# Kernel tuning notes

Hardware: AMD Instinct MI355X
Metric: run time of the kernel (lower is better)

Reference implementation:

```python
import jax, jax.numpy as jnp
import numpy as np

PATCH = 16  # conv kernel size == stride


def _patch_embed(im, W, b):
    # im: (B, C, H, W) NCHW; W: (hidden, C, s, s); returns (B, h, w, hidden)
    out = jax.lax.conv_general_dilated(
        im, W, window_strides=(PATCH, PATCH), padding='VALID',
        dimension_numbers=('NCHW', 'OIHW', 'NCHW'))
    out = out + b[None, :, None, None]
    return jnp.transpose(out, (0, 2, 3, 1))  # (B, h, w, hidden)


def setup_inputs() -> dict:
    key = jax.random.key(0)
    k1, k2, k3, k4 = jax.random.split(key, 4)
    B, C, H, Wd = 64, 3, 224, 224
    hidden = 384
    x = jax.random.normal(k1, (B, C, H, Wd), dtype=jnp.float32)
    y = jax.random.normal(k2, (B, C, H, Wd), dtype=jnp.float32)
    fan_in = C * PATCH * PATCH
    bound = 1.0 / np.sqrt(fan_in)
    W = jax.random.uniform(k3, (hidden, C, PATCH, PATCH), dtype=jnp.float32,
                           minval=-bound, maxval=bound)
    b = jax.random.uniform(k4, (hidden,), dtype=jnp.float32,
                           minval=-bound, maxval=bound)
    return {'x': x, 'y': y, 'W': W, 'b': b}


def reference(x, y, W, b):
    B = x.shape[0]
    xp = _patch_embed(x, W, b)  # (B, h, w, C)
    yp = _patch_embed(y, W, b)  # (B, h, w, C)
    h, w = xp.shape[1], xp.shape[2]
    logp = jax.nn.log_softmax(xp, axis=-1)          # (B, h, w, C)
    q = jax.lax.stop_gradient(jax.nn.softmax(yp, axis=-1))  # detached targets
    # CE[i, j] = mean over (h, w) of -(q_j * logp_i).sum(-1)
    # Faithful factorization of the (B, B, h, w, C) broadcast in the original.
    CE = -jnp.einsum('ihwc,jhwc->ij', logp, q) / (h * w)  # (B, B)
    close = jnp.trace(CE) / B
    far = (CE.sum() - jnp.trace(CE)) / (B * B - B)
    return close / far
```

## Files before the change

### kernel.cpp

```cpp
#include <hip/hip_runtime.h>

#define HID   384
#define K_PE  768
#define IMGST 150528

typedef unsigned short ushort_t;
using f32x4  = __attribute__((ext_vector_type(4))) float;
using short8 = __attribute__((ext_vector_type(8))) short;

__device__ __forceinline__ unsigned bfpack(float lo, float hi) {
    union { float f; unsigned u; } a, b; a.f = lo; b.f = hi;
    unsigned ra = (a.u + 0x7fffu + ((a.u >> 16) & 1u)) >> 16;
    unsigned rb = (b.u + 0x7fffu + ((b.u >> 16) & 1u)) & 0xffff0000u;
    return ra | rb;
}

__global__ __launch_bounds__(256) void prep(const float* __restrict__ W,
                                            ushort_t* __restrict__ Wfrag,
                                            float* __restrict__ scal) {
    const int t = blockIdx.x * 256 + threadIdx.x;
    if (t < 4) scal[t] = 0.f;
    const int n  = t / 96;
    const int ko = t % 96;
    const float4 a = *(const float4*)(W + (size_t)n * K_PE + ko * 8);
    const float4 b = *(const float4*)(W + (size_t)n * K_PE + ko * 8 + 4);
    uint4 p;
    p.x = bfpack(a.x, a.y); p.y = bfpack(a.z, a.w);
    p.z = bfpack(b.x, b.y); p.w = bfpack(b.z, b.w);
    const int nt   = n >> 4;
    const int kc   = ko >> 2;
    const int lane = (ko & 3) * 16 + (n & 15);
    ((uint4*)Wfrag)[(nt * 24 + kc) * 64 + lane] = p;
}

__global__ __launch_bounds__(512, 2) void pe_all(
    const float* __restrict__ xin, const float* __restrict__ yin,
    const ushort_t* __restrict__ Wfrag, const float* __restrict__ bias,
    float* __restrict__ scal, float* __restrict__ out) {
    const int p  = blockIdx.x;
    const int pi = p / 14;
    const int pj = p - pi * 14;

    __shared__ __align__(16) ushort_t Asx[2][64 * 64];
    __shared__ __align__(16) ushort_t Asy[2][64 * 64];
    __shared__ float Smx[8][32], Ssx[8][32], Smy[8][32], Ssy[8][32];
    __shared__ float LcL[2][HID], LcQ[2][HID];
    __shared__ float sT[8], sS[8];

    const int tid  = threadIdx.x;
    const int wave = tid >> 6;
    const int lane = tid & 63;
    const int lm   = lane & 15;
    const int lq   = lane >> 4;
    const int mg   = wave >> 2;
    const int nw   = wave & 3;
    const int wn   = nw * 96;

    const int sm = tid >> 3;
    const int qt = tid & 7;
    const float* abx = xin + (size_t)sm * IMGST + pi * 3584 + pj * 16;
    const float* aby = yin + (size_t)sm * IMGST + pi * 3584 + pj * 16;
    const int awoff = sm * 64 + ((qt ^ (sm & 7)) * 8);

    int ard[2][2];
#pragma unroll
    for (int ks = 0; ks < 2; ++ks)
#pragma unroll
        for (int mi = 0; mi < 2; ++mi)
            ard[ks][mi] = (mg * 32 + mi * 16 + lm) * 64 +
                          (((ks * 4 + lq) ^ (lm & 7)) * 8);

    const ushort_t* bbase = Wfrag + (size_t)lane * 8;

    f32x4 accx[2][6] = {};
    f32x4 accy[2][6] = {};

#define STAGE(KB, BUF)                                                       \
    {                                                                        \
        const int k0  = (KB) + qt * 8;                                       \
        const int off = (k0 >> 8) * 50176 + (((k0 >> 4) & 15) * 224) + (k0 & 15); \
        float4 f0 = *(const float4*)(abx + off);                             \
        float4 f1 = *(const float4*)(abx + off + 4);                         \
        float4 g0 = *(const float4*)(aby + off);                             \
        float4 g1 = *(const float4*)(aby + off + 4);                         \
        uint4 px, py;                                                        \
        px.x = bfpack(f0.x, f0.y); px.y = bfpack(f0.z, f0.w);                \
        px.z = bfpack(f1.x, f1.y); px.w = bfpack(f1.z, f1.w);                \
        py.x = bfpack(g0.x, g0.y); py.y = bfpack(g0.z, g0.w);                \
        py.z = bfpack(g1.x, g1.y); py.w = bfpack(g1.z, g1.w);                \
        *(uint4*)&Asx[BUF][awoff] = px;                                      \
        *(uint4*)&Asy[BUF][awoff] = py;                                      \
    }

    STAGE(0, 0)
    __syncthreads();

    for (int kbi = 0; kbi < 12; ++kbi) {
        const int cur = kbi & 1;
        if (kbi < 11) STAGE(kbi * 64 + 64, cur ^ 1)
#pragma unroll
        for (int ks = 0; ks < 2; ++ks) {
            short8 bfr[6], afx[2], afy[2];
#pragma unroll
            for (int ni = 0; ni < 6; ++ni)
                bfr[ni] = *(const short8*)(bbase +
                          (size_t)(((nw * 6 + ni) * 24 + kbi * 2 + ks) * 64) * 8);
#pragma unroll
            for (int mi = 0; mi < 2; ++mi) {
                afx[mi] = *(const short8*)&Asx[cur][ard[ks][mi]];
                afy[mi] = *(const short8*)&Asy[cur][ard[ks][mi]];
            }
#pragma unroll
            for (int mi = 0; mi < 2; ++mi)
#pragma unroll
                for (int ni = 0; ni < 6; ++ni) {
                    accx[mi][ni] = __builtin_amdgcn_mfma_f32_16x16x32_bf16(
                        afx[mi], bfr[ni], accx[mi][ni], 0, 0, 0);
                    accy[mi][ni] = __builtin_amdgcn_mfma_f32_16x16x32_bf16(
                        afy[mi], bfr[ni], accy[mi][ni], 0, 0, 0);
                }
        }
        __syncthreads();
    }
#undef STAGE

#pragma unroll
    for (int ni = 0; ni < 6; ++ni) {
        const float bv = bias[wn + ni * 16 + lm];
#pragma unroll
        for (int mi = 0; mi < 2; ++mi)
#pragma unroll
            for (int r = 0; r < 4; ++r) {
                accx[mi][ni][r] += bv;
                accy[mi][ni][r] += bv;
            }
    }

    float mx[2][4], my_[2][4];
#pragma unroll
    for (int mi = 0; mi < 2; ++mi)
#pragma unroll
        for (int r = 0; r < 4; ++r) {
            float a = accx[mi][0][r], b = accy[mi][0][r];
#pragma unroll
            for (int ni = 1; ni < 6; ++ni) {
                a = fmaxf(a, accx[mi][ni][r]);
                b = fmaxf(b, accy[mi][ni][r]);
            }
            mx[mi][r] = a; my_[mi][r] = b;
        }
#pragma unroll
    for (int off = 1; off < 16; off <<= 1)
#pragma unroll
        for (int mi = 0; mi < 2; ++mi)
#pragma unroll
            for (int r = 0; r < 4; ++r) {
                mx[mi][r]  = fmaxf(mx[mi][r],  __shfl_xor(mx[mi][r],  off));
                my_[mi][r] = fmaxf(my_[mi][r], __shfl_xor(my_[mi][r], off));
            }
    if (lm == 0)
#pragma unroll
        for (int mi = 0; mi < 2; ++mi)
#pragma unroll
            for (int r = 0; r < 4; ++r) {
                Smx[wave][mi * 16 + lq * 4 + r] = mx[mi][r];
                Smy[wave][mi * 16 + lq * 4 + r] = my_[mi][r];
            }
    __syncthreads();
#pragma unroll
    for (int mi = 0; mi < 2; ++mi)
#pragma unroll
        for (int r = 0; r < 4; ++r) {
            const int row = mi * 16 + lq * 4 + r;
            mx[mi][r]  = fmaxf(fmaxf(Smx[mg * 4 + 0][row], Smx[mg * 4 + 1][row]),
                               fmaxf(Smx[mg * 4 + 2][row], Smx[mg * 4 + 3][row]));
            my_[mi][r] = fmaxf(fmaxf(Smy[mg * 4 + 0][row], Smy[mg * 4 + 1][row]),
                               fmaxf(Smy[mg * 4 + 2][row], Smy[mg * 4 + 3][row]));
        }

    float sx[2][4], sy[2][4];
#pragma unroll
    for (int mi = 0; mi < 2; ++mi)
#pragma unroll
        for (int r = 0; r < 4; ++r) {
            float a = 0.f, b = 0.f;
#pragma unroll
            for (int ni = 0; ni < 6; ++ni) {
                a += __expf(accx[mi][ni][r] - mx[mi][r]);
                b += __expf(accy[mi][ni][r] - my_[mi][r]);
            }
            sx[mi][r] = a; sy[mi][r] = b;
        }
#pragma unroll
    for (int off = 1; off < 16; off <<= 1)
#pragma unroll
        for (int mi = 0; mi < 2; ++mi)
#pragma unroll
            for (int r = 0; r < 4; ++r) {
                sx[mi][r] += __shfl_xor(sx[mi][r], off);
                sy[mi][r] += __shfl_xor(sy[mi][r], off);
            }
    if (lm == 0)
#pragma unroll
        for (int mi = 0; mi < 2; ++mi)
#pragma unroll
            for (int r = 0; r < 4; ++r) {
                Ssx[wave][mi * 16 + lq * 4 + r] = sx[mi][r];
                Ssy[wave][mi * 16 + lq * 4 + r] = sy[mi][r];
            }
    __syncthreads();
#pragma unroll
    for (int mi = 0; mi < 2; ++mi)
#pragma unroll
        for (int r = 0; r < 4; ++r) {
            const int row = mi * 16 + lq * 4 + r;
            const float ssx = Ssx[mg * 4 + 0][row] + Ssx[mg * 4 + 1][row] +
                              Ssx[mg * 4 + 2][row] + Ssx[mg * 4 + 3][row];
            const float ssy = Ssy[mg * 4 + 0][row] + Ssy[mg * 4 + 1][row] +
                              Ssy[mg * 4 + 2][row] + Ssy[mg * 4 + 3][row];
            sx[mi][r] = mx[mi][r] + __logf(ssx);
            sy[mi][r] = 1.f / ssy;
        }

    float T = 0.f;
    float cL[6], cQ[6];
#pragma unroll
    for (int ni = 0; ni < 6; ++ni) { cL[ni] = 0.f; cQ[ni] = 0.f; }
#pragma unroll
    for (int mi = 0; mi < 2; ++mi)
#pragma unroll
        for (int r = 0; r < 4; ++r) {
            const float sh  = sx[mi][r];
            const float m   = my_[mi][r];
            const float inv = sy[mi][r];
#pragma unroll
            for (int ni = 0; ni < 6; ++ni) {
                const float lp = accx[mi][ni][r] - sh;
                const float qv = __expf(accy[mi][ni][r] - m) * inv;
                T += lp * qv;
                cL[ni] += lp;
                cQ[ni] += qv;
            }
        }
#pragma unroll
    for (int ni = 0; ni < 6; ++ni) {
        cL[ni] += __shfl_xor(cL[ni], 16); cL[ni] += __shfl_xor(cL[ni], 32);
        cQ[ni] += __shfl_xor(cQ[ni], 16); cQ[ni] += __shfl_xor(cQ[ni], 32);
    }
    if (lq == 0)
#pragma unroll
        for (int ni = 0; ni < 6; ++ni) {
            LcL[mg][wn + ni * 16 + lm] = cL[ni];
            LcQ[mg][wn + ni * 16 + lm] = cQ[ni];
        }
#pragma unroll
    for (int off = 32; off > 0; off >>= 1) T += __shfl_xor(T, off);
    if (lane == 0) sT[wave] = T;
    __syncthreads();

    float sp = 0.f;
    if (tid < HID) {
        const float L = LcL[0][tid] + LcL[1][tid];
        const float Q = LcQ[0][tid] + LcQ[1][tid];
        sp = L * Q;
    }
#pragma unroll
    for (int off = 32; off > 0; off >>= 1) sp += __shfl_xor(sp, off);
    if (lane == 0) sS[wave] = sp;
    __syncthreads();

    if (tid == 0) {
        float Tb = sT[0] + sT[1] + sT[2] + sT[3] + sT[4] + sT[5] + sT[6] + sT[7];
        float Sb = sS[0] + sS[1] + sS[2] + sS[3] + sS[4] + sS[5] + sS[6] + sS[7];
        atomicAdd(&scal[0], Tb);
        atomicAdd(&scal[1], Sb);
        __threadfence();
        int old = atomicAdd((int*)&scal[3], 1);
        if (old == (int)gridDim.x - 1) {
            float Tt = atomicAdd(&scal[0], 0.f);
            float St = atomicAdd(&scal[1], 0.f);
            out[0] = 63.f * Tt / (St - Tt);
        }
    }
}

extern "C" void kernel_launch(void* const* d_in, const int* in_sizes, int n_in,
                              void* d_out, int out_size, void* d_ws, size_t ws_size,
                              hipStream_t stream) {
    const float* x = (const float*)d_in[0];
    const float* y = (const float*)d_in[1];
    const float* W = (const float*)d_in[2];
    const float* b = (const float*)d_in[3];
    float* out = (float*)d_out;

    float*    scal  = (float*)d_ws;
    ushort_t* Wfrag = (ushort_t*)(scal + 16);

    prep<<<144, 256, 0, stream>>>(W, Wfrag, scal);
    pe_all<<<196, 512, 0, stream>>>(x, y, Wfrag, b, scal, out);
}
```

Measured before the change: 145.6 us.

## Split batch across blocks with atomic column sums and a final dot kernel

The batch of 64 images is split into four groups of 16, giving a 196x4 grid of 256-thread blocks instead of 196 blocks of 512 threads. Each block adds its per-patch column sums of log-probabilities and targets into global arrays with atomics. A third kernel then computes the sum of their products and the final ratio. This raises parallelism and occupancy across the device, at the cost of global atomic traffic, an extra launch, and reloading the weight fragments four times as often.

```diff
diff --git a/kernel.cpp b/kernel.cpp
--- a/kernel.cpp
+++ b/kernel.cpp
@@ -3,6 +3,7 @@
 #define HID   384
 #define K_PE  768
 #define IMGST 150528
+#define NCOLS 75264
 
 typedef unsigned short ushort_t;
 using f32x4  = __attribute__((ext_vector_type(4))) float;
@@ -17,79 +18,78 @@
 
 __global__ __launch_bounds__(256) void prep(const float* __restrict__ W,
                                             ushort_t* __restrict__ Wfrag,
-                                            float* __restrict__ scal) {
+                                            float* __restrict__ scal,
+                                            float* __restrict__ Lsum,
+                                            float* __restrict__ Qsum) {
     const int t = blockIdx.x * 256 + threadIdx.x;
     if (t < 4) scal[t] = 0.f;
-    const int n  = t / 96;
-    const int ko = t % 96;
-    const float4 a = *(const float4*)(W + (size_t)n * K_PE + ko * 8);
-    const float4 b = *(const float4*)(W + (size_t)n * K_PE + ko * 8 + 4);
-    uint4 p;
-    p.x = bfpack(a.x, a.y); p.y = bfpack(a.z, a.w);
-    p.z = bfpack(b.x, b.y); p.w = bfpack(b.z, b.w);
-    const int nt   = n >> 4;
-    const int kc   = ko >> 2;
-    const int lane = (ko & 3) * 16 + (n & 15);
-    ((uint4*)Wfrag)[(nt * 24 + kc) * 64 + lane] = p;
-}
-
-__global__ __launch_bounds__(512, 2) void pe_all(
+    if (t < NCOLS / 4) {
+        ((float4*)Lsum)[t] = float4{0.f, 0.f, 0.f, 0.f};
+        ((float4*)Qsum)[t] = float4{0.f, 0.f, 0.f, 0.f};
+    }
+    if (t < 36864) {
+        const int n  = t / 96;
+        const int ko = t % 96;
+        const float4 a = *(const float4*)(W + (size_t)n * K_PE + ko * 8);
+        const float4 b = *(const float4*)(W + (size_t)n * K_PE + ko * 8 + 4);
+        uint4 p;
+        p.x = bfpack(a.x, a.y); p.y = bfpack(a.z, a.w);
+        p.z = bfpack(b.x, b.y); p.w = bfpack(b.z, b.w);
+        const int nt   = n >> 4;
+        const int kc   = ko >> 2;
+        const int lane = (ko & 3) * 16 + (n & 15);
+        ((uint4*)Wfrag)[(nt * 24 + kc) * 64 + lane] = p;
+    }
+}
+
+__global__ __launch_bounds__(256, 4) void pe_all(
     const float* __restrict__ xin, const float* __restrict__ yin,
     const ushort_t* __restrict__ Wfrag, const float* __restrict__ bias,
-    float* __restrict__ scal, float* __restrict__ out) {
+    float* __restrict__ scal, float* __restrict__ Lsum,
+    float* __restrict__ Qsum) {
     const int p  = blockIdx.x;
+    const int ig = blockIdx.y;
     const int pi = p / 14;
     const int pj = p - pi * 14;
 
-    __shared__ __align__(16) ushort_t Asx[2][64 * 64];
-    __shared__ __align__(16) ushort_t Asy[2][64 * 64];
-    __shared__ float Smx[8][32], Ssx[8][32], Smy[8][32], Ssy[8][32];
-    __shared__ float LcL[2][HID], LcQ[2][HID];
-    __shared__ float sT[8], sS[8];
+    __shared__ __align__(16) ushort_t As[2][2][16 * 64];
+    __shared__ float Smx[4][16], Ssx[4][16], Smy[4][16], Ssy[4][16];
+    __shared__ float sT[4];
 
     const int tid  = threadIdx.x;
     const int wave = tid >> 6;
     const int lane = tid & 63;
     const int lm   = lane & 15;
     const int lq   = lane >> 4;
-    const int mg   = wave >> 2;
-    const int nw   = wave & 3;
-    const int wn   = nw * 96;
-
-    const int sm = tid >> 3;
+    const int wn   = wave * 96;
+
+    const int z  = tid >> 7;
+    const int sm = (tid >> 3) & 15;
     const int qt = tid & 7;
-    const float* abx = xin + (size_t)sm * IMGST + pi * 3584 + pj * 16;
-    const float* aby = yin + (size_t)sm * IMGST + pi * 3584 + pj * 16;
-    const int awoff = sm * 64 + ((qt ^ (sm & 7)) * 8);
-
-    int ard[2][2];
+    const float* ab = (z ? yin : xin) +
+                      (size_t)(ig * 16 + sm) * IMGST + pi * 3584 + pj * 16;
+    ushort_t* awp = &As[z][0][sm * 64 + ((qt ^ (sm & 7)) * 8)];
+
+    int ard[2];
 #pragma unroll
     for (int ks = 0; ks < 2; ++ks)
-#pragma unroll
-        for (int mi = 0; mi < 2; ++mi)
-            ard[ks][mi] = (mg * 32 + mi * 16 + lm) * 64 +
-                          (((ks * 4 + lq) ^ (lm & 7)) * 8);
+        ard[ks] = lm * 64 + (((ks * 4 + lq) ^ (lm & 7)) * 8);
 
     const ushort_t* bbase = Wfrag + (size_t)lane * 8;
 
-    f32x4 accx[2][6] = {};
-    f32x4 accy[2][6] = {};
+    f32x4 accx[6] = {};
+    f32x4 accy[6] = {};
 
 #define STAGE(KB, BUF)                                                       \
     {                                                                        \
         const int k0  = (KB) + qt * 8;                                       \
         const int off = (k0 >> 8) * 50176 + (((k0 >> 4) & 15) * 224) + (k0 & 15); \
-        float4 f0 = *(const float4*)(abx + off);                             \
-        float4 f1 = *(const float4*)(abx + off + 4);                         \
-        float4 g0 = *(const float4*)(aby + off);                             \
-        float4 g1 = *(const float4*)(aby + off + 4);                         \
-        uint4 px, py;                                                        \
+        float4 f0 = *(const float4*)(ab + off);                              \
+        float4 f1 = *(const float4*)(ab + off + 4);                          \
+        uint4 px;                                                            \
         px.x = bfpack(f0.x, f0.y); px.y = bfpack(f0.z, f0.w);                \
         px.z = bfpack(f1.x, f1.y); px.w = bfpack(f1.z, f1.w);                \
-        py.x = bfpack(g0.x, g0.y); py.y = bfpack(g0.z, g0.w);                \
-        py.z = bfpack(g1.x, g1.y); py.w = bfpack(g1.z, g1.w);                \
-        *(uint4*)&Asx[BUF][awoff] = px;                                      \
-        *(uint4*)&Asy[BUF][awoff] = py;                                      \
+        *(uint4*)(awp + (BUF) * 1024) = px;                                  \
     }
 
     STAGE(0, 0)
@@ -100,25 +100,20 @@
         if (kbi < 11) STAGE(kbi * 64 + 64, cur ^ 1)
 #pragma unroll
         for (int ks = 0; ks < 2; ++ks) {
-            short8 bfr[6], afx[2], afy[2];
+            short8 bfr[6];
 #pragma unroll
             for (int ni = 0; ni < 6; ++ni)
                 bfr[ni] = *(const short8*)(bbase +
-                          (size_t)(((nw * 6 + ni) * 24 + kbi * 2 + ks) * 64) * 8);
-#pragma unroll
-            for (int mi = 0; mi < 2; ++mi) {
-                afx[mi] = *(const short8*)&Asx[cur][ard[ks][mi]];
-                afy[mi] = *(const short8*)&Asy[cur][ard[ks][mi]];
+                          (size_t)(((wave * 6 + ni) * 24 + kbi * 2 + ks) * 64) * 8);
+            short8 afx = *(const short8*)&As[0][cur][ard[ks]];
+            short8 afy = *(const short8*)&As[1][cur][ard[ks]];
+#pragma unroll
+            for (int ni = 0; ni < 6; ++ni) {
+                accx[ni] = __builtin_amdgcn_mfma_f32_16x16x32_bf16(
+                    afx, bfr[ni], accx[ni], 0, 0, 0);
+                accy[ni] = __builtin_amdgcn_mfma_f32_16x16x32_bf16(
+                    afy, bfr[ni], accy[ni], 0, 0, 0);
             }
-#pragma unroll
-            for (int mi = 0; mi < 2; ++mi)
-#pragma unroll
-                for (int ni = 0; ni < 6; ++ni) {
-                    accx[mi][ni] = __builtin_amdgcn_mfma_f32_16x16x32_bf16(
-                        afx[mi], bfr[ni], accx[mi][ni], 0, 0, 0);
-                    accy[mi][ni] = __builtin_amdgcn_mfma_f32_16x16x32_bf16(
-                        afy[mi], bfr[ni], accy[mi][ni], 0, 0, 0);
-                }
         }
         __syncthreads();
     }
@@ -128,120 +123,98 @@
     for (int ni = 0; ni < 6; ++ni) {
         const float bv = bias[wn + ni * 16 + lm];
 #pragma unroll
-        for (int mi = 0; mi < 2; ++mi)
-#pragma unroll
-            for (int r = 0; r < 4; ++r) {
-                accx[mi][ni][r] += bv;
-                accy[mi][ni][r] += bv;
-            }
-    }
-
-    float mx[2][4], my_[2][4];
-#pragma unroll
-    for (int mi = 0; mi < 2; ++mi)
-#pragma unroll
-        for (int r = 0; r < 4; ++r) {
-            float a = accx[mi][0][r], b = accy[mi][0][r];
-#pragma unroll
-            for (int ni = 1; ni < 6; ++ni) {
-                a = fmaxf(a, accx[mi][ni][r]);
-                b = fmaxf(b, accy[mi][ni][r]);
-            }
-            mx[mi][r] = a; my_[mi][r] = b;
-        }
+        for (int r = 0; r < 4; ++r) {
+            accx[ni][r] += bv;
+            accy[ni][r] += bv;
+        }
+    }
+
+    float mx[4], my_[4];
+#pragma unroll
+    for (int r = 0; r < 4; ++r) {
+        float a = accx[0][r], b = accy[0][r];
+#pragma unroll
+        for (int ni = 1; ni < 6; ++ni) {
+            a = fmaxf(a, accx[ni][r]);
+            b = fmaxf(b, accy[ni][r]);
+        }
+        mx[r] = a; my_[r] = b;
+    }
 #pragma unroll
     for (int off = 1; off < 16; off <<= 1)
 #pragma unroll
-        for (int mi = 0; mi < 2; ++mi)
-#pragma unroll
-            for (int r = 0; r < 4; ++r) {
-                mx[mi][r]  = fmaxf(mx[mi][r],  __shfl_xor(mx[mi][r],  off));
-                my_[mi][r] = fmaxf(my_[mi][r], __shfl_xor(my_[mi][r], off));
-            }
+        for (int r = 0; r < 4; ++r) {
+            mx[r]  = fmaxf(mx[r],  __shfl_xor(mx[r],  off));
+            my_[r] = fmaxf(my_[r], __shfl_xor(my_[r], off));
+        }
     if (lm == 0)
 #pragma unroll
-        for (int mi = 0; mi < 2; ++mi)
-#pragma unroll
-            for (int r = 0; r < 4; ++r) {
-                Smx[wave][mi * 16 + lq * 4 + r] = mx[mi][r];
-                Smy[wave][mi * 16 + lq * 4 + r] = my_[mi][r];
-            }
-    __syncthreads();
-#pragma unroll
-    for (int mi = 0; mi < 2; ++mi)
-#pragma unroll
-        for (int r = 0; r < 4; ++r) {
-            const int row = mi * 16 + lq * 4 + r;
-            mx[mi][r]  = fmaxf(fmaxf(Smx[mg * 4 + 0][row], Smx[mg * 4 + 1][row]),
-                               fmaxf(Smx[mg * 4 + 2][row], Smx[mg * 4 + 3][row]));
-            my_[mi][r] = fmaxf(fmaxf(Smy[mg * 4 + 0][row], Smy[mg * 4 + 1][row]),
-                               fmaxf(Smy[mg * 4 + 2][row], Smy[mg * 4 + 3][row]));
-        }
-
-    float sx[2][4], sy[2][4];
-#pragma unroll
-    for (int mi = 0; mi < 2; ++mi)
-#pragma unroll
-        for (int r = 0; r < 4; ++r) {
-            float a = 0.f, b = 0.f;
-#pragma unroll
-            for (int ni = 0; ni < 6; ++ni) {
-                a += __expf(accx[mi][ni][r] - mx[mi][r]);
-                b += __expf(accy[mi][ni][r] - my_[mi][r]);
-            }
-            sx[mi][r] = a; sy[mi][r] = b;
-        }
+        for (int r = 0; r < 4; ++r) {
+            Smx[wave][lq * 4 + r] = mx[r];
+            Smy[wave][lq * 4 + r] = my_[r];
+        }
+    __syncthreads();
+#pragma unroll
+    for (int r = 0; r < 4; ++r) {
+        const int row = lq * 4 + r;
+        mx[r]  = fmaxf(fmaxf(Smx[0][row], Smx[1][row]),
+                       fmaxf(Smx[2][row], Smx[3][row]));
+        my_[r] = fmaxf(fmaxf(Smy[0][row], Smy[1][row]),
+                       fmaxf(Smy[2][row], Smy[3][row]));
+    }
+
+    float sx[4], sy[4];
+#pragma unroll
+    for (int r = 0; r < 4; ++r) {
+        float a = 0.f, b = 0.f;
+#pragma unroll
+        for (int ni = 0; ni < 6; ++ni) {
+            a += __expf(accx[ni][r] - mx[r]);
+            b += __expf(accy[ni][r] - my_[r]);
+        }
+        sx[r] = a; sy[r] = b;
+    }
 #pragma unroll
     for (int off = 1; off < 16; off <<= 1)
 #pragma unroll
-        for (int mi = 0; mi < 2; ++mi)
-#pragma unroll
-            for (int r = 0; r < 4; ++r) {
-                sx[mi][r] += __shfl_xor(sx[mi][r], off);
-                sy[mi][r] += __shfl_xor(sy[mi][r], off);
-            }
+        for (int r = 0; r < 4; ++r) {
+            sx[r] += __shfl_xor(sx[r], off);
+            sy[r] += __shfl_xor(sy[r], off);
+        }
     if (lm == 0)
 #pragma unroll
-        for (int mi = 0; mi < 2; ++mi)
-#pragma unroll
-            for (int r = 0; r < 4; ++r) {
-                Ssx[wave][mi * 16 + lq * 4 + r] = sx[mi][r];
-                Ssy[wave][mi * 16 + lq * 4 + r] = sy[mi][r];
-            }
-    __syncthreads();
-#pragma unroll
-    for (int mi = 0; mi < 2; ++mi)
-#pragma unroll
-        for (int r = 0; r < 4; ++r) {
-            const int row = mi * 16 + lq * 4 + r;
-            const float ssx = Ssx[mg * 4 + 0][row] + Ssx[mg * 4 + 1][row] +
-                              Ssx[mg * 4 + 2][row] + Ssx[mg * 4 + 3][row];
-            const float ssy = Ssy[mg * 4 + 0][row] + Ssy[mg * 4 + 1][row] +
-                              Ssy[mg * 4 + 2][row] + Ssy[mg * 4 + 3][row];
-            sx[mi][r] = mx[mi][r] + __logf(ssx);
-            sy[mi][r] = 1.f / ssy;
-        }
+        for (int r = 0; r < 4; ++r) {
+            Ssx[wave][lq * 4 + r] = sx[r];
+            Ssy[wave][lq * 4 + r] = sy[r];
+        }
+    __syncthreads();
+#pragma unroll
+    for (int r = 0; r < 4; ++r) {
+        const int row = lq * 4 + r;
+        const float ssx = Ssx[0][row] + Ssx[1][row] + Ssx[2][row] + Ssx[3][row];
+        const float ssy = Ssy[0][row] + Ssy[1][row] + Ssy[2][row] + Ssy[3][row];
+        sx[r] = mx[r] + __logf(ssx);
+        sy[r] = 1.f / ssy;
+    }
 
     float T = 0.f;
     float cL[6], cQ[6];
 #pragma unroll
     for (int ni = 0; ni < 6; ++ni) { cL[ni] = 0.f; cQ[ni] = 0.f; }
 #pragma unroll
-    for (int mi = 0; mi < 2; ++mi)
-#pragma unroll
-        for (int r = 0; r < 4; ++r) {
-            const float sh  = sx[mi][r];
-            const float m   = my_[mi][r];
-            const float inv = sy[mi][r];
-#pragma unroll
-            for (int ni = 0; ni < 6; ++ni) {
-                const float lp = accx[mi][ni][r] - sh;
-                const float qv = __expf(accy[mi][ni][r] - m) * inv;
-                T += lp * qv;
-                cL[ni] += lp;
-                cQ[ni] += qv;
-            }
-        }
+    for (int r = 0; r < 4; ++r) {
+        const float sh  = sx[r];
+        const float m   = my_[r];
+        const float inv = sy[r];
+#pragma unroll
+        for (int ni = 0; ni < 6; ++ni) {
+            const float lp = accx[ni][r] - sh;
+            const float qv = __expf(accy[ni][r] - m) * inv;
+            T += lp * qv;
+            cL[ni] += lp;
+            cQ[ni] += qv;
+        }
+    }
 #pragma unroll
     for (int ni = 0; ni < 6; ++ni) {
         cL[ni] += __shfl_xor(cL[ni], 16); cL[ni] += __shfl_xor(cL[ni], 32);
@@ -250,37 +223,46 @@
     if (lq == 0)
 #pragma unroll
         for (int ni = 0; ni < 6; ++ni) {
-            LcL[mg][wn + ni * 16 + lm] = cL[ni];
-            LcQ[mg][wn + ni * 16 + lm] = cQ[ni];
+            const int col = p * HID + wn + ni * 16 + lm;
+            atomicAdd(&Lsum[col], cL[ni]);
+            atomicAdd(&Qsum[col], cQ[ni]);
         }
 #pragma unroll
     for (int off = 32; off > 0; off >>= 1) T += __shfl_xor(T, off);
     if (lane == 0) sT[wave] = T;
     __syncthreads();
-
-    float sp = 0.f;
-    if (tid < HID) {
-        const float L = LcL[0][tid] + LcL[1][tid];
-        const float Q = LcQ[0][tid] + LcQ[1][tid];
-        sp = L * Q;
-    }
-#pragma unroll
-    for (int off = 32; off > 0; off >>= 1) sp += __shfl_xor(sp, off);
-    if (lane == 0) sS[wave] = sp;
-    __syncthreads();
-
-    if (tid == 0) {
-        float Tb = sT[0] + sT[1] + sT[2] + sT[3] + sT[4] + sT[5] + sT[6] + sT[7];
-        float Sb = sS[0] + sS[1] + sS[2] + sS[3] + sS[4] + sS[5] + sS[6] + sS[7];
-        atomicAdd(&scal[0], Tb);
-        atomicAdd(&scal[1], Sb);
+    if (tid == 0)
+        atomicAdd(&scal[0], sT[0] + sT[1] + sT[2] + sT[3]);
+}
+
+__global__ __launch_bounds__(256) void final_dot(const float* __restrict__ Lsum,
+                                                 const float* __restrict__ Qsum,
+                                                 float* __restrict__ scal,
+                                                 float* __restrict__ out) {
+    const int idx = blockIdx.x * 256 + threadIdx.x;
+    float s = 0.f;
+    if (idx < NCOLS / 4) {
+        float4 a = ((const float4*)Lsum)[idx];
+        float4 b = ((const float4*)Qsum)[idx];
+        s = a.x * b.x + a.y * b.y + a.z * b.z + a.w * b.w;
+    }
+#pragma unroll
+    for (int off = 32; off > 0; off >>= 1) s += __shfl_xor(s, off);
+    __shared__ float sS[4];
+    __shared__ int lastflag;
+    if ((threadIdx.x & 63) == 0) sS[threadIdx.x >> 6] = s;
+    __syncthreads();
+    if (threadIdx.x == 0) {
+        atomicAdd(&scal[1], sS[0] + sS[1] + sS[2] + sS[3]);
         __threadfence();
         int old = atomicAdd((int*)&scal[3], 1);
-        if (old == (int)gridDim.x - 1) {
-            float Tt = atomicAdd(&scal[0], 0.f);
-            float St = atomicAdd(&scal[1], 0.f);
-            out[0] = 63.f * Tt / (St - Tt);
-        }
+        lastflag = (old == (int)gridDim.x - 1);
+    }
+    __syncthreads();
+    if (lastflag && threadIdx.x == 0) {
+        float S = atomicAdd(&scal[1], 0.f);
+        float T = atomicAdd(&scal[0], 0.f);
+        out[0] = 63.f * T / (S - T);
     }
 }
 
@@ -294,8 +276,11 @@
     float* out = (float*)d_out;
 
     float*    scal  = (float*)d_ws;
-    ushort_t* Wfrag = (ushort_t*)(scal + 16);
-
-    prep<<<144, 256, 0, stream>>>(W, Wfrag, scal);
-    pe_all<<<196, 512, 0, stream>>>(x, y, Wfrag, b, scal, out);
-}
+    float*    Lsum  = scal + 16;
+    float*    Qsum  = Lsum + NCOLS;
+    ushort_t* Wfrag = (ushort_t*)(Qsum + NCOLS);
+
+    prep<<<148, 256, 0, stream>>>(W, Wfrag, scal, Lsum, Qsum);
+    pe_all<<<dim3(196, 4), 256, 0, stream>>>(x, y, Wfrag, b, scal, Lsum, Qsum);
+    final_dot<<<74, 256, 0, stream>>>(Lsum, Qsum, scal, out);
+}
```

After: 154.6 us. +6.1%, slower.
